# Kernel optimization log

Measured on AMD Instinct MI355X. Metric: run time of the kernel, lower is better.

Reference implementation:

```python
import jax, jax.numpy as jnp
import numpy as np

EMBED = 768
HEADS = 8
HEAD_DIM = EMBED // HEADS
DEPTH = 12
MLP_H = 4 * EMBED
N_PATCH = 1568  # (16/2) * (224/16)^2
N_CLASSES = 1000
EPS = 1e-5


def _pos_encoding(num_pos, num_dims):
    j = np.arange(num_dims)
    angle = np.arange(num_pos)[:, None] / np.power(10000.0, 2.0 * (j // 2) / num_dims)[None, :]
    table = angle.copy()
    table[:, 0::2] = np.sin(angle[:, 0::2])
    table[:, 1::2] = np.cos(angle[:, 1::2])
    return jnp.asarray(table[None], dtype=jnp.float32)  # [1, N, C]

POS = _pos_encoding(N_PATCH, EMBED)


def ln(x, scale, bias):
    m = x.mean(-1, keepdims=True)
    v = jnp.var(x, axis=-1, keepdims=True)
    return (x - m) / jnp.sqrt(v + EPS) * scale + bias


def setup_inputs() -> dict:
    key = jax.random.key(0)
    ks = jax.random.split(key, 8)
    B = 2
    f = lambda k, shape: jax.random.normal(k, shape, dtype=jnp.float32) * 0.02
    return {
        "x": jax.random.normal(ks[0], (B, 3, 16, 224, 224), dtype=jnp.float32),
        "conv_w": f(ks[1], (EMBED, 3, 2, 16, 16)),
        "conv_b": jnp.zeros((EMBED,), jnp.float32),
        "norm1_scale": jnp.ones((DEPTH, EMBED), jnp.float32),
        "norm1_bias": jnp.zeros((DEPTH, EMBED), jnp.float32),
        "qkv_w": f(ks[2], (DEPTH, 3 * EMBED, EMBED)),
        "out_w": f(ks[3], (DEPTH, EMBED, EMBED)),
        "out_b": jnp.zeros((DEPTH, EMBED), jnp.float32),
        "norm2_scale": jnp.ones((DEPTH, EMBED), jnp.float32),
        "norm2_bias": jnp.zeros((DEPTH, EMBED), jnp.float32),
        "fc1_w": f(ks[4], (DEPTH, MLP_H, EMBED)),
        "fc1_b": jnp.zeros((DEPTH, MLP_H), jnp.float32),
        "fc2_w": f(ks[5], (DEPTH, EMBED, MLP_H)),
        "fc2_b": jnp.zeros((DEPTH, EMBED), jnp.float32),
        "fc_norm_scale": jnp.ones((EMBED,), jnp.float32),
        "fc_norm_bias": jnp.zeros((EMBED,), jnp.float32),
        "head_w": f(ks[6], (N_CLASSES, EMBED)),
        "head_b": jnp.zeros((N_CLASSES,), jnp.float32),
    }


def reference(x, conv_w, conv_b, norm1_scale, norm1_bias, qkv_w, out_w, out_b,
              norm2_scale, norm2_bias, fc1_w, fc1_b, fc2_w, fc2_b,
              fc_norm_scale, fc_norm_bias, head_w, head_b):
    B = x.shape[0]
    # tubelet patch embed: Conv3d stride == kernel == (2,16,16)
    h = jax.lax.conv_general_dilated(
        x, conv_w, window_strides=(2, 16, 16), padding='VALID',
        dimension_numbers=('NCDHW', 'OIDHW', 'NCDHW'))
    h = h + conv_b[None, :, None, None, None]
    h = h.reshape(B, EMBED, -1).transpose(0, 2, 1)  # [B, N, C]
    h = h + POS

    def blk(h, p):
        n1s, n1b, qw, ow, ob, n2s, n2b, w1, b1, w2, b2 = p
        y = ln(h, n1s, n1b)
        qkv = (y @ qw.T).reshape(B, N_PATCH, 3, HEADS, HEAD_DIM)
        q, k, v = jnp.moveaxis(qkv, 2, 0)  # each [B, N, H, d]
        # NOTE: source applies NO 1/sqrt(d) scaling
        attn = jax.nn.softmax(jnp.einsum('bnhd,bmhd->bhnm', q, k), axis=-1)
        o = jnp.einsum('bhnm,bmhd->bnhd', attn, v).reshape(B, N_PATCH, EMBED)
        h = h + o @ ow.T + ob
        y = ln(h, n2s, n2b)
        y = jax.nn.gelu(y @ w1.T + b1, approximate=False) @ w2.T + b2
        return h + y, None

    params = (norm1_scale, norm1_bias, qkv_w, out_w, out_b,
              norm2_scale, norm2_bias, fc1_w, fc1_b, fc2_w, fc2_b)
    h, _ = jax.lax.scan(blk, h, params)

    pooled = ln(h.mean(1), fc_norm_scale, fc_norm_bias)
    return pooled @ head_w.T + head_b
```

## Files before the change

kernel.cpp:

```cpp
#include <hip/hip_runtime.h>
#include <math.h>

#define EMBED 768
#define NPATCH 1568
#define BB 2
#define MROWS (BB * NPATCH)
#define HEADS 8
#define MLPH 3072
#define DEPTH 12

#define F_BIAS 1
#define F_GELU 2
#define F_RES  4
#define F_POS  8

typedef unsigned short u16;
typedef __bf16 bf16x8 __attribute__((ext_vector_type(8)));
typedef float floatx4 __attribute__((ext_vector_type(4)));
typedef unsigned int u32x4 __attribute__((ext_vector_type(4)));
typedef unsigned short u16x4 __attribute__((ext_vector_type(4)));

__device__ inline u16 f2bf(float f) {
  union { float f; unsigned int u; } v; v.f = f;
  unsigned int u = v.u;
  u += 0x7fffu + ((u >> 16) & 1u);
  return (u16)(u >> 16);
}
__device__ inline void st_out(float* p, float v) { *p = v; }
__device__ inline void st_out(u16* p, float v) { *p = f2bf(v); }

__global__ __launch_bounds__(256) void castw(const float* __restrict__ src,
                                             u16* __restrict__ dst, int n4) {
  int i = blockIdx.x * 256 + threadIdx.x;
  if (i >= n4) return;
  float4 v = ((const float4*)src)[i];
  u16x4 o; o.x = f2bf(v.x); o.y = f2bf(v.y); o.z = f2bf(v.z); o.w = f2bf(v.w);
  ((u16x4*)dst)[i] = o;
}

__global__ __launch_bounds__(256) void vit_im2col(const float* __restrict__ x,
                                                  u16* __restrict__ col) {
  int idx = blockIdx.x * 256 + threadIdx.x;
  const int total = MROWS * 384;
  if (idx >= total) return;
  int k4 = idx % 384, row = idx / 384;
  int k = k4 * 4;
  int b = row / NPATCH, n = row % NPATCH;
  int dz = n / 196; int rem = n - dz * 196; int hy = rem / 14; int wx = rem - hy * 14;
  int ci = k >> 9; int kr = k & 511; int kd = kr >> 8; int kr2 = kr & 255;
  int kh = kr2 >> 4; int kw = kr2 & 15;
  const float* src = x + ((((size_t)b * 3 + ci) * 16 + (dz * 2 + kd)) * 224 +
                          (hy * 16 + kh)) * 224 + (wx * 16 + kw);
  float4 v = *(const float4*)src;
  u16x4 o; o.x = f2bf(v.x); o.y = f2bf(v.y); o.z = f2bf(v.z); o.w = f2bf(v.w);
  *(u16x4*)(col + (size_t)row * 1536 + k) = o;
}

__device__ inline float pos_embed_val(int n, int c) {
  double e = (double)(2 * (c >> 1)) / 768.0;
  double ang = (double)n / pow(10000.0, e);
  return (float)((c & 1) ? cos(ang) : sin(ang));
}

template <int FLAGS, typename OT>
__global__ __launch_bounds__(256) void mfma_gemm(const u16* __restrict__ A,
                                                 const u16* __restrict__ W,
                                                 const float* __restrict__ bias,
                                                 OT* __restrict__ C,
                                                 const float* __restrict__ Res,
                                                 int Mr, int Nout, int K) {
  __shared__ u16 As[128 * 56] __attribute__((aligned(16)));
  __shared__ u16 Bs[128 * 56] __attribute__((aligned(16)));
  const int tid = threadIdx.x;
  const int m0 = blockIdx.y * 128, n0 = blockIdx.x * 128;
  const int lane = tid & 63, w = tid >> 6;
  const int wr = w >> 1, wc = w & 1;
  const int l15 = lane & 15, quad = lane >> 4;

  const int srow = tid >> 2, skoff = (tid & 3) * 8;
  int ar0 = m0 + srow;      if (ar0 > Mr - 1) ar0 = Mr - 1;
  int ar1 = m0 + 64 + srow; if (ar1 > Mr - 1) ar1 = Mr - 1;
  const u16* Ap0 = A + (size_t)ar0 * K + skoff;
  const u16* Ap1 = A + (size_t)ar1 * K + skoff;
  const u16* Bp0 = W + (size_t)(n0 + srow) * K + skoff;
  const u16* Bp1 = W + (size_t)(n0 + 64 + srow) * K + skoff;
  u16* Asw = As + srow * 56 + skoff;
  u16* Bsw = Bs + srow * 56 + skoff;

  floatx4 acc[4][4];
#pragma unroll
  for (int i = 0; i < 4; i++)
#pragma unroll
    for (int j = 0; j < 4; j++) acc[i][j] = (floatx4){0.f, 0.f, 0.f, 0.f};

  u32x4 ga0 = *(const u32x4*)Ap0, ga1 = *(const u32x4*)Ap1;
  u32x4 gb0 = *(const u32x4*)Bp0, gb1 = *(const u32x4*)Bp1;

  for (int k0 = 0; k0 < K; k0 += 32) {
    __syncthreads();
    *(u32x4*)Asw = ga0; *(u32x4*)(Asw + 64 * 56) = ga1;
    *(u32x4*)Bsw = gb0; *(u32x4*)(Bsw + 64 * 56) = gb1;
    __syncthreads();
    int kn = k0 + 32;
    if (kn < K) {
      ga0 = *(const u32x4*)(Ap0 + kn); ga1 = *(const u32x4*)(Ap1 + kn);
      gb0 = *(const u32x4*)(Bp0 + kn); gb1 = *(const u32x4*)(Bp1 + kn);
    }
    bf16x8 af[4], bfr[4];
#pragma unroll
    for (int i = 0; i < 4; i++)
      af[i] = *(const bf16x8*)(As + (wr * 64 + i * 16 + l15) * 56 + quad * 8);
#pragma unroll
    for (int j = 0; j < 4; j++)
      bfr[j] = *(const bf16x8*)(Bs + (wc * 64 + j * 16 + l15) * 56 + quad * 8);
#pragma unroll
    for (int i = 0; i < 4; i++)
#pragma unroll
      for (int j = 0; j < 4; j++)
        acc[i][j] = __builtin_amdgcn_mfma_f32_16x16x32_bf16(af[i], bfr[j], acc[i][j], 0, 0, 0);
  }

#pragma unroll
  for (int i = 0; i < 4; i++) {
#pragma unroll
    for (int j = 0; j < 4; j++) {
      int col = n0 + wc * 64 + j * 16 + l15;
#pragma unroll
      for (int r = 0; r < 4; r++) {
        int row = m0 + wr * 64 + i * 16 + quad * 4 + r;
        if (row >= Mr) continue;
        float v = acc[i][j][r];
        if (FLAGS & F_BIAS) v += bias[col];
        if (FLAGS & F_GELU) v = 0.5f * v * (1.f + erff(v * 0.70710678118654752f));
        if (FLAGS & F_POS)  v += pos_embed_val(row % NPATCH, col);
        if (FLAGS & F_RES)  v += Res[(size_t)row * Nout + col];
        st_out(C + (size_t)row * Nout + col, v);
      }
    }
  }
}

template <typename OT>
__global__ __launch_bounds__(256) void vit_ln(const float* __restrict__ X,
                                              OT* __restrict__ Y,
                                              const float* __restrict__ scale,
                                              const float* __restrict__ bias) {
  const int row = blockIdx.x;
  const float* x = X + (size_t)row * EMBED;
  const int t = threadIdx.x;
  float v0 = x[t], v1 = x[t + 256], v2 = x[t + 512];
  float s = v0 + v1 + v2;
  float s2 = v0 * v0 + v1 * v1 + v2 * v2;
#pragma unroll
  for (int off = 32; off > 0; off >>= 1) {
    s += __shfl_down(s, off);
    s2 += __shfl_down(s2, off);
  }
  __shared__ float red[8];
  __shared__ float stats[2];
  int wid = t >> 6, lane = t & 63;
  if (lane == 0) { red[wid] = s; red[4 + wid] = s2; }
  __syncthreads();
  if (t == 0) {
    float S = red[0] + red[1] + red[2] + red[3];
    float S2 = red[4] + red[5] + red[6] + red[7];
    float mean = S * (1.f / 768.f);
    float var = S2 * (1.f / 768.f) - mean * mean;
    stats[0] = mean; stats[1] = rsqrtf(var + 1e-5f);
  }
  __syncthreads();
  float mean = stats[0], rstd = stats[1];
  OT* y = Y + (size_t)row * EMBED;
  st_out(y + t,       (v0 - mean) * rstd * scale[t]       + bias[t]);
  st_out(y + t + 256, (v1 - mean) * rstd * scale[t + 256] + bias[t + 256]);
  st_out(y + t + 512, (v2 - mean) * rstd * scale[t + 512] + bias[t + 512]);
}

__global__ __launch_bounds__(128) void vtrans(const u16* __restrict__ qkvb,
                                              u16* __restrict__ Vt) {
  __shared__ u16 T[32][48] __attribute__((aligned(16)));
  int bx = blockIdx.x, by = blockIdx.y, bh = blockIdx.z;
  int b = bh >> 3, h = bh & 7;
  int t = threadIdx.x;
  int r = t >> 2, c = (t & 3) * 8;
  int n = bx * 32 + r;
  const u16* src = qkvb + ((size_t)(b * NPATCH + n)) * 2304 + 1536 + h * 96 + by * 32 + c;
  *(u32x4*)&T[r][c] = *(const u32x4*)src;
  __syncthreads();
  u16 tmp[8];
#pragma unroll
  for (int j = 0; j < 8; j++) tmp[j] = T[c + j][r];
  u16* dst = Vt + (size_t)bh * 96 * NPATCH + (size_t)(by * 32 + r) * NPATCH + bx * 32 + c;
  *(u32x4*)dst = *(u32x4*)tmp;
}

__global__ __launch_bounds__(256) void vit_attn(const u16* __restrict__ qkvb,
                                                const u16* __restrict__ Vt,
                                                u16* __restrict__ O) {
  __shared__ u16 Ks[32 * 104] __attribute__((aligned(16)));
  __shared__ u16 Vs[96 * 56]  __attribute__((aligned(16)));
  __shared__ u16 Ps[4][16 * 56] __attribute__((aligned(16)));
  const int tid = threadIdx.x;
  const int w = tid >> 6, lane = tid & 63;
  const int l15 = lane & 15, quad = lane >> 4;
  const int bh = blockIdx.y, b = bh >> 3, hh = bh & 7;
  const int q0 = blockIdx.x * 64;
  const size_t qbase = (size_t)b * NPATCH * 2304 + (size_t)hh * 96;
  const size_t kbase = qbase + 768;
  const size_t vtb = (size_t)bh * 96 * NPATCH;

  bf16x8 qf[3];
  {
    int gq = q0 + w * 16 + l15; if (gq > NPATCH - 1) gq = NPATCH - 1;
    const u16* qp = qkvb + qbase + (size_t)gq * 2304 + quad * 8;
    qf[0] = *(const bf16x8*)(qp);
    qf[1] = *(const bf16x8*)(qp + 32);
    qf[2] = *(const bf16x8*)(qp + 64);
  }

  floatx4 of[6];
#pragma unroll
  for (int dc = 0; dc < 6; dc++) of[dc] = (floatx4){0.f, 0.f, 0.f, 0.f};
  float m_r[4] = {-INFINITY, -INFINITY, -INFINITY, -INFINITY};
  float l_r[4] = {0.f, 0.f, 0.f, 0.f};
  u16* pw = &Ps[w][0];

  for (int kt = 0; kt < NPATCH; kt += 32) {
    __syncthreads();
    for (int idx = tid; idx < 384; idx += 256) {
      int r = idx / 12, c8 = idx % 12;
      *(u32x4*)(Ks + r * 104 + c8 * 8) =
          *(const u32x4*)(qkvb + kbase + (size_t)(kt + r) * 2304 + c8 * 8);
    }
    for (int idx = tid; idx < 384; idx += 256) {
      int d = idx >> 2, c8 = idx & 3;
      *(u32x4*)(Vs + d * 56 + c8 * 8) =
          *(const u32x4*)(Vt + vtb + (size_t)d * NPATCH + kt + c8 * 8);
    }
    __syncthreads();

    floatx4 sf0 = (floatx4){0.f, 0.f, 0.f, 0.f};
    floatx4 sf1 = (floatx4){0.f, 0.f, 0.f, 0.f};
#pragma unroll
    for (int kc = 0; kc < 3; kc++) {
      bf16x8 kf0 = *(const bf16x8*)(Ks + l15 * 104 + kc * 32 + quad * 8);
      bf16x8 kf1 = *(const bf16x8*)(Ks + (16 + l15) * 104 + kc * 32 + quad * 8);
      sf0 = __builtin_amdgcn_mfma_f32_16x16x32_bf16(qf[kc], kf0, sf0, 0, 0, 0);
      sf1 = __builtin_amdgcn_mfma_f32_16x16x32_bf16(qf[kc], kf1, sf1, 0, 0, 0);
    }

    float alpha[4], p0[4], p1[4];
#pragma unroll
    for (int r = 0; r < 4; r++) {
      float t = fmaxf(sf0[r], sf1[r]);
      t = fmaxf(t, __shfl_xor(t, 1));
      t = fmaxf(t, __shfl_xor(t, 2));
      t = fmaxf(t, __shfl_xor(t, 4));
      t = fmaxf(t, __shfl_xor(t, 8));
      float mnew = fmaxf(m_r[r], t);
      alpha[r] = __expf(m_r[r] - mnew);
      m_r[r] = mnew;
      p0[r] = __expf(sf0[r] - mnew);
      p1[r] = __expf(sf1[r] - mnew);
      float rs = p0[r] + p1[r];
      rs += __shfl_xor(rs, 1);
      rs += __shfl_xor(rs, 2);
      rs += __shfl_xor(rs, 4);
      rs += __shfl_xor(rs, 8);
      l_r[r] = l_r[r] * alpha[r] + rs;
    }
#pragma unroll
    for (int r = 0; r < 4; r++) {
      pw[(quad * 4 + r) * 56 + l15] = f2bf(p0[r]);
      pw[(quad * 4 + r) * 56 + 16 + l15] = f2bf(p1[r]);
    }
    bf16x8 af = *(const bf16x8*)(pw + l15 * 56 + quad * 8);
#pragma unroll
    for (int dc = 0; dc < 6; dc++) {
      bf16x8 vf = *(const bf16x8*)(Vs + (dc * 16 + l15) * 56 + quad * 8);
      floatx4 o = of[dc];
#pragma unroll
      for (int r = 0; r < 4; r++) o[r] *= alpha[r];
      of[dc] = __builtin_amdgcn_mfma_f32_16x16x32_bf16(af, vf, o, 0, 0, 0);
    }
  }

  float inv_l[4];
#pragma unroll
  for (int r = 0; r < 4; r++) inv_l[r] = 1.f / l_r[r];
  const int gqb = q0 + w * 16 + quad * 4;
#pragma unroll
  for (int dc = 0; dc < 6; dc++) {
#pragma unroll
    for (int r = 0; r < 4; r++) {
      int gq = gqb + r;
      if (gq < NPATCH)
        O[(size_t)(b * NPATCH + gq) * EMBED + hh * 96 + dc * 16 + l15] =
            f2bf(of[dc][r] * inv_l[r]);
    }
  }
}

__global__ __launch_bounds__(256) void vit_colmean(const float* __restrict__ h,
                                                   float* __restrict__ pooled) {
  int c = blockIdx.x * 256 + threadIdx.x;
  int b = blockIdx.y;
  const float* p = h + (size_t)b * NPATCH * EMBED + c;
  float s = 0.f;
  for (int n = 0; n < NPATCH; n++) s += p[(size_t)n * EMBED];
  pooled[b * EMBED + c] = s * (1.f / (float)NPATCH);
}

__global__ __launch_bounds__(256) void vit_head(const float* __restrict__ pooled,
                                                const float* __restrict__ hw,
                                                const float* __restrict__ hb,
                                                float* __restrict__ out) {
  int gw = (blockIdx.x * 256 + threadIdx.x) >> 6;
  int lane = threadIdx.x & 63;
  if (gw >= 2000) return;
  int b = gw / 1000, cls = gw % 1000;
  const float* p = pooled + b * EMBED;
  const float* wv = hw + (size_t)cls * EMBED;
  float s = 0.f;
  for (int j = lane; j < EMBED; j += 64) s = fmaf(p[j], wv[j], s);
#pragma unroll
  for (int off = 32; off > 0; off >>= 1) s += __shfl_down(s, off);
  if (lane == 0) out[gw] = s + hb[cls];
}

extern "C" void kernel_launch(void* const* d_in, const int* in_sizes, int n_in,
                              void* d_out, int out_size, void* d_ws, size_t ws_size,
                              hipStream_t stream) {
  const float* x      = (const float*)d_in[0];
  const float* conv_w = (const float*)d_in[1];
  const float* conv_b = (const float*)d_in[2];
  const float* n1s    = (const float*)d_in[3];
  const float* n1b    = (const float*)d_in[4];
  const float* qkv_w  = (const float*)d_in[5];
  const float* out_w  = (const float*)d_in[6];
  const float* out_b  = (const float*)d_in[7];
  const float* n2s    = (const float*)d_in[8];
  const float* n2b    = (const float*)d_in[9];
  const float* fc1_w  = (const float*)d_in[10];
  const float* fc1_b  = (const float*)d_in[11];
  const float* fc2_w  = (const float*)d_in[12];
  const float* fc2_b  = (const float*)d_in[13];
  const float* fns    = (const float*)d_in[14];
  const float* fnb    = (const float*)d_in[15];
  const float* head_w = (const float*)d_in[16];
  const float* head_b = (const float*)d_in[17];
  float* out = (float*)d_out;

  char* ws = (char*)d_ws;
  float* h      = (float*)ws;
  u16*   qkvb   = (u16*)(ws + 9633792);
  u16*   regB   = (u16*)(ws + 24084480);
  u16*   ybf    = regB;
  u16*   attnout= regB;
  u16*   mlpb   = regB + (size_t)MROWS * EMBED;
  u16*   im2c   = regB;
  u16*   Vt     = (u16*)(ws + 48168960);
  u16*   wbuf   = (u16*)(ws + 52985856);
  float* pooled = (float*)(ws + 57704448);
  float* pooled2= pooled + BB * EMBED;

  vit_im2col<<<(MROWS * 384 + 255) / 256, 256, 0, stream>>>(x, im2c);
  castw<<<(1536 * 768 / 4 + 255) / 256, 256, 0, stream>>>(conv_w, wbuf, 1536 * 768 / 4);
  mfma_gemm<F_BIAS | F_POS, float><<<dim3(6, 25), 256, 0, stream>>>(
      im2c, wbuf, conv_b, h, nullptr, MROWS, 768, 1536);

  for (int l = 0; l < DEPTH; l++) {
    vit_ln<u16><<<MROWS, 256, 0, stream>>>(h, ybf, n1s + l * EMBED, n1b + l * EMBED);
    castw<<<(2304 * 768 / 4 + 255) / 256, 256, 0, stream>>>(
        qkv_w + (size_t)l * 2304 * 768, wbuf, 2304 * 768 / 4);
    mfma_gemm<0, u16><<<dim3(18, 25), 256, 0, stream>>>(
        ybf, wbuf, nullptr, qkvb, nullptr, MROWS, 2304, 768);
    vtrans<<<dim3(49, 3, 16), 128, 0, stream>>>(qkvb, Vt);
    vit_attn<<<dim3(25, 16), 256, 0, stream>>>(qkvb, Vt, attnout);
    castw<<<(768 * 768 / 4 + 255) / 256, 256, 0, stream>>>(
        out_w + (size_t)l * 768 * 768, wbuf, 768 * 768 / 4);
    mfma_gemm<F_BIAS | F_RES, float><<<dim3(6, 25), 256, 0, stream>>>(
        attnout, wbuf, out_b + l * EMBED, h, h, MROWS, 768, 768);
    vit_ln<u16><<<MROWS, 256, 0, stream>>>(h, ybf, n2s + l * EMBED, n2b + l * EMBED);
    castw<<<(3072 * 768 / 4 + 255) / 256, 256, 0, stream>>>(
        fc1_w + (size_t)l * 3072 * 768, wbuf, 3072 * 768 / 4);
    mfma_gemm<F_BIAS | F_GELU, u16><<<dim3(24, 25), 256, 0, stream>>>(
        ybf, wbuf, fc1_b + l * MLPH, mlpb, nullptr, MROWS, 3072, 768);
    castw<<<(768 * 3072 / 4 + 255) / 256, 256, 0, stream>>>(
        fc2_w + (size_t)l * 768 * 3072, wbuf, 768 * 3072 / 4);
    mfma_gemm<F_BIAS | F_RES, float><<<dim3(6, 25), 256, 0, stream>>>(
        mlpb, wbuf, fc2_b + l * EMBED, h, h, MROWS, 768, 3072);
  }

  vit_colmean<<<dim3(3, BB), 256, 0, stream>>>(h, pooled);
  vit_ln<float><<<BB, 256, 0, stream>>>(pooled, pooled2, fns, fnb);
  vit_head<<<500, 256, 0, stream>>>(pooled2, head_w, head_b, out);
}
```

Baseline: 4.315 ms.

## Split-K the N=768 GEMMs with narrower tiles and a fused reduce epilogue

Replaces the 128x128-tile GEMM used for the patch-embed, out-projection and fc2 layers with a 128x64-tile split-K (2-way) kernel that writes fp32 partials. A separate vectorized reduce kernel then sums the partials and applies bias, positional encoding or residual. This raises the block count from 150 to 600 so all compute units get work. It costs extra partial-buffer traffic and an additional kernel launch per GEMM. The workspace layout is rearranged so the partial buffer reuses the qkv and V-transpose regions.

```diff
diff --git a/kernel.cpp b/kernel.cpp
--- a/kernel.cpp
+++ b/kernel.cpp
@@ -132,12 +132,114 @@
         float v = acc[i][j][r];
         if (FLAGS & F_BIAS) v += bias[col];
         if (FLAGS & F_GELU) v = 0.5f * v * (1.f + erff(v * 0.70710678118654752f));
-        if (FLAGS & F_POS)  v += pos_embed_val(row % NPATCH, col);
         if (FLAGS & F_RES)  v += Res[(size_t)row * Nout + col];
         st_out(C + (size_t)row * Nout + col, v);
       }
     }
   }
+}
+
+__global__ __launch_bounds__(256) void mfma_gemm_split(const u16* __restrict__ A,
+                                                       const u16* __restrict__ W,
+                                                       float* __restrict__ P,
+                                                       int Mr, int Nout, int K, int Kc) {
+  __shared__ u16 As[128 * 56] __attribute__((aligned(16)));
+  __shared__ u16 Bs[64 * 56]  __attribute__((aligned(16)));
+  const int tid = threadIdx.x;
+  const int m0 = blockIdx.y * 128, n0 = blockIdx.x * 64;
+  const int z = blockIdx.z;
+  const int lane = tid & 63, w = tid >> 6;
+  const int wr = w >> 1, wc = w & 1;
+  const int l15 = lane & 15, quad = lane >> 4;
+
+  const int srow = tid >> 2, skoff = (tid & 3) * 8;
+  int ar0 = m0 + srow;      if (ar0 > Mr - 1) ar0 = Mr - 1;
+  int ar1 = m0 + 64 + srow; if (ar1 > Mr - 1) ar1 = Mr - 1;
+  const u16* Ap0 = A + (size_t)ar0 * K + skoff;
+  const u16* Ap1 = A + (size_t)ar1 * K + skoff;
+  const u16* Bp  = W + (size_t)(n0 + srow) * K + skoff;
+  u16* Asw = As + srow * 56 + skoff;
+  u16* Bsw = Bs + srow * 56 + skoff;
+
+  floatx4 acc[4][2];
+#pragma unroll
+  for (int i = 0; i < 4; i++)
+#pragma unroll
+    for (int j = 0; j < 2; j++) acc[i][j] = (floatx4){0.f, 0.f, 0.f, 0.f};
+
+  const int kb = z * Kc, ke = kb + Kc;
+  u32x4 ga0 = *(const u32x4*)(Ap0 + kb), ga1 = *(const u32x4*)(Ap1 + kb);
+  u32x4 gb = *(const u32x4*)(Bp + kb);
+
+  for (int k0 = kb; k0 < ke; k0 += 32) {
+    __syncthreads();
+    *(u32x4*)Asw = ga0; *(u32x4*)(Asw + 64 * 56) = ga1;
+    if (srow < 64) *(u32x4*)Bsw = gb;
+    __syncthreads();
+    int kn = k0 + 32;
+    if (kn < ke) {
+      ga0 = *(const u32x4*)(Ap0 + kn); ga1 = *(const u32x4*)(Ap1 + kn);
+      gb = *(const u32x4*)(Bp + kn);
+    }
+    bf16x8 af[4], bfr[2];
+#pragma unroll
+    for (int i = 0; i < 4; i++)
+      af[i] = *(const bf16x8*)(As + (wr * 64 + i * 16 + l15) * 56 + quad * 8);
+#pragma unroll
+    for (int j = 0; j < 2; j++)
+      bfr[j] = *(const bf16x8*)(Bs + (wc * 32 + j * 16 + l15) * 56 + quad * 8);
+#pragma unroll
+    for (int i = 0; i < 4; i++)
+#pragma unroll
+      for (int j = 0; j < 2; j++)
+        acc[i][j] = __builtin_amdgcn_mfma_f32_16x16x32_bf16(af[i], bfr[j], acc[i][j], 0, 0, 0);
+  }
+
+  float* Pz = P + (size_t)z * Mr * Nout;
+#pragma unroll
+  for (int i = 0; i < 4; i++) {
+#pragma unroll
+    for (int j = 0; j < 2; j++) {
+      int col = n0 + wc * 32 + j * 16 + l15;
+#pragma unroll
+      for (int r = 0; r < 4; r++) {
+        int row = m0 + wr * 64 + i * 16 + quad * 4 + r;
+        if (row < Mr) Pz[(size_t)row * Nout + col] = acc[i][j][r];
+      }
+    }
+  }
+}
+
+template <int FLAGS>
+__global__ __launch_bounds__(256) void reduce_split(const float* __restrict__ P, int S,
+                                                    const float* __restrict__ bias,
+                                                    const float* __restrict__ Res,
+                                                    float* __restrict__ Out,
+                                                    int n4, int Nout) {
+  int i = blockIdx.x * 256 + threadIdx.x;
+  if (i >= n4) return;
+  const float4* p4 = (const float4*)P;
+  float4 a = p4[i];
+  for (int zz = 1; zz < S; zz++) {
+    float4 b = p4[i + (size_t)zz * n4];
+    a.x += b.x; a.y += b.y; a.z += b.z; a.w += b.w;
+  }
+  int col = (i * 4) % Nout;
+  if (FLAGS & F_BIAS) {
+    a.x += bias[col]; a.y += bias[col + 1]; a.z += bias[col + 2]; a.w += bias[col + 3];
+  }
+  if (FLAGS & F_POS) {
+    int n = ((i * 4) / Nout) % NPATCH;
+    a.x += pos_embed_val(n, col);
+    a.y += pos_embed_val(n, col + 1);
+    a.z += pos_embed_val(n, col + 2);
+    a.w += pos_embed_val(n, col + 3);
+  }
+  if (FLAGS & F_RES) {
+    float4 r4 = ((const float4*)Res)[i];
+    a.x += r4.x; a.y += r4.y; a.z += r4.z; a.w += r4.w;
+  }
+  ((float4*)Out)[i] = a;
 }
 
 template <typename OT>
@@ -354,20 +456,24 @@
   char* ws = (char*)d_ws;
   float* h      = (float*)ws;
   u16*   qkvb   = (u16*)(ws + 9633792);
-  u16*   regB   = (u16*)(ws + 24084480);
+  u16*   Vt     = (u16*)(ws + 24084480);
+  float* P      = (float*)(ws + 9633792);
+  u16*   regB   = (u16*)(ws + 28901376);
   u16*   ybf    = regB;
   u16*   attnout= regB;
+  u16*   im2c   = regB;
   u16*   mlpb   = regB + (size_t)MROWS * EMBED;
-  u16*   im2c   = regB;
-  u16*   Vt     = (u16*)(ws + 48168960);
   u16*   wbuf   = (u16*)(ws + 52985856);
   float* pooled = (float*)(ws + 57704448);
   float* pooled2= pooled + BB * EMBED;
 
+  const int n4 = MROWS * EMBED / 4;
+
   vit_im2col<<<(MROWS * 384 + 255) / 256, 256, 0, stream>>>(x, im2c);
   castw<<<(1536 * 768 / 4 + 255) / 256, 256, 0, stream>>>(conv_w, wbuf, 1536 * 768 / 4);
-  mfma_gemm<F_BIAS | F_POS, float><<<dim3(6, 25), 256, 0, stream>>>(
-      im2c, wbuf, conv_b, h, nullptr, MROWS, 768, 1536);
+  mfma_gemm_split<<<dim3(12, 25, 2), 256, 0, stream>>>(im2c, wbuf, P, MROWS, 768, 1536, 768);
+  reduce_split<F_BIAS | F_POS><<<(n4 + 255) / 256, 256, 0, stream>>>(
+      P, 2, conv_b, nullptr, h, n4, 768);
 
   for (int l = 0; l < DEPTH; l++) {
     vit_ln<u16><<<MROWS, 256, 0, stream>>>(h, ybf, n1s + l * EMBED, n1b + l * EMBED);
@@ -379,8 +485,9 @@
     vit_attn<<<dim3(25, 16), 256, 0, stream>>>(qkvb, Vt, attnout);
     castw<<<(768 * 768 / 4 + 255) / 256, 256, 0, stream>>>(
         out_w + (size_t)l * 768 * 768, wbuf, 768 * 768 / 4);
-    mfma_gemm<F_BIAS | F_RES, float><<<dim3(6, 25), 256, 0, stream>>>(
-        attnout, wbuf, out_b + l * EMBED, h, h, MROWS, 768, 768);
+    mfma_gemm_split<<<dim3(12, 25, 2), 256, 0, stream>>>(attnout, wbuf, P, MROWS, 768, 768, 384);
+    reduce_split<F_BIAS | F_RES><<<(n4 + 255) / 256, 256, 0, stream>>>(
+        P, 2, out_b + l * EMBED, h, h, n4, 768);
     vit_ln<u16><<<MROWS, 256, 0, stream>>>(h, ybf, n2s + l * EMBED, n2b + l * EMBED);
     castw<<<(3072 * 768 / 4 + 255) / 256, 256, 0, stream>>>(
         fc1_w + (size_t)l * 3072 * 768, wbuf, 3072 * 768 / 4);
@@ -388,8 +495,9 @@
         ybf, wbuf, fc1_b + l * MLPH, mlpb, nullptr, MROWS, 3072, 768);
     castw<<<(768 * 3072 / 4 + 255) / 256, 256, 0, stream>>>(
         fc2_w + (size_t)l * 768 * 3072, wbuf, 768 * 3072 / 4);
-    mfma_gemm<F_BIAS | F_RES, float><<<dim3(6, 25), 256, 0, stream>>>(
-        mlpb, wbuf, fc2_b + l * EMBED, h, h, MROWS, 768, 3072);
+    mfma_gemm_split<<<dim3(12, 25, 2), 256, 0, stream>>>(mlpb, wbuf, P, MROWS, 768, 3072, 1536);
+    reduce_split<F_BIAS | F_RES><<<(n4 + 255) / 256, 256, 0, stream>>>(
+        P, 2, fc2_b + l * EMBED, h, h, n4, 768);
   }
 
   vit_colmean<<<dim3(3, BB), 256, 0, stream>>>(h, pooled);
```

Result: faster. 3.770 ms (-12.6%).
